# Optimization experiments

Measured on AMD Instinct MI355X. Metric: run time of the kernel, lower is better.

## Reference

```python
import jax, jax.numpy as jnp
import numpy as np


def setup_inputs() -> dict:
    key = jax.random.key(0)
    ks = jax.random.split(key, 7)
    B, C, H, W = 8, 1024, 64, 64
    heads, head_dim, red = 8, 128, 8
    s = 1.0 / np.sqrt(head_dim)
    return {
        "x": jax.random.normal(ks[0], (B, C, H, W), jnp.float32),
        "Wq": jax.random.normal(ks[1], (heads, red, head_dim), jnp.float32) * s,
        "bq": jax.random.normal(ks[2], (heads, red), jnp.float32) * s,
        "Wk": jax.random.normal(ks[3], (heads, red, head_dim), jnp.float32) * s,
        "bk": jax.random.normal(ks[4], (heads, red), jnp.float32) * s,
        "Wv": jax.random.normal(ks[5], (heads, head_dim, head_dim), jnp.float32) * s,
        "bv": jax.random.normal(ks[6], (heads, head_dim), jnp.float32) * s,
    }


def reference(x, Wq, bq, Wk, bk, Wv, bv):
    B, C, H, W = x.shape
    heads, red, d = Wq.shape  # d = head_dim
    # (B, heads, head_dim, HW)
    xh = x.reshape(B, heads, d, H * W)
    # per-head spatial average pool: (B, heads, head_dim)
    avg = jnp.mean(xh, axis=-1)
    # torch Linear: y = x @ W.T + b, applied per head
    q = jnp.einsum("bhds,hrd->bhsr", xh, Wq) + bq[None, :, None, :]   # (B,H,S,r)
    k = jnp.einsum("bhd,hrd->bhr", avg, Wk) + bk[None]                 # (B,H,r)
    v = jnp.einsum("bhd,hed->bhe", avg, Wv) + bv[None]                 # (B,H,d)
    # single-key attention; softmax over the spatial dim (torch dim=1)
    scores = jnp.einsum("bhsr,bhr->bhs", q, k)                          # (B,H,S)
    attn = jax.nn.softmax(scores, axis=-1)
    out = jnp.einsum("bhs,bhe->bhes", attn, v)                          # (B,H,d,S)
    return out.reshape(B, C, H, W)
```

## Files before the change

### kernel.cpp

```cpp
#include <hip/hip_runtime.h>
#include <math.h>

#define SDIM 4096
#define DDIM 128
#define RED 8
#define BATCH 8
#define BH 64
#define CH 1024

typedef float vfloat4 __attribute__((ext_vector_type(4)));

#define WS_V   8192
#define WS_SC  16384

__inline__ __device__ float wave_reduce_sum(float v) {
#pragma unroll
    for (int o = 32; o > 0; o >>= 1) v += __shfl_down(v, o, 64);
    return v;
}
__inline__ __device__ float wave_reduce_max(float v) {
#pragma unroll
    for (int o = 32; o > 0; o >>= 1) v = fmaxf(v, __shfl_down(v, o, 64));
    return v;
}

__global__ __launch_bounds__(256) void k_avg(const float* __restrict__ x,
                                             float* __restrict__ ws) {
    const int row = blockIdx.x;
    const int t = threadIdx.x;
    const float4* xr = (const float4*)(x + (size_t)row * SDIM);
    float s = 0.f;
#pragma unroll
    for (int p = 0; p < 4; ++p) {
        float4 v = xr[t + 256 * p];
        s += v.x + v.y + v.z + v.w;
    }
    s = wave_reduce_sum(s);
    __shared__ float part[4];
    const int wave = t >> 6, lane = t & 63;
    if (lane == 0) part[wave] = s;
    __syncthreads();
    if (t == 0) {
        float tot = part[0] + part[1] + part[2] + part[3];
        ws[row] = tot * (1.0f / SDIM);
    }
}

__global__ __launch_bounds__(256) void k_scores(
        const float* __restrict__ x,
        const float* __restrict__ Wq, const float* __restrict__ bq,
        const float* __restrict__ Wk, const float* __restrict__ bk,
        float* __restrict__ ws) {
    const int blk = blockIdx.x;
    const int bh = blk >> 3, chunk = blk & 7;
    const int b = bh >> 3, h = bh & 7;
    const int t = threadIdx.x;

    __shared__ float avgs[DDIM];
    __shared__ float kk[RED];
    __shared__ float wqs[DDIM];
    __shared__ float cc;

    if (t < DDIM) avgs[t] = ws[b * CH + h * DDIM + t];
    __syncthreads();
    if (t < RED) {
        const float* wkr = Wk + (h * RED + t) * DDIM;
        float acc = 0.f;
#pragma unroll 8
        for (int d = 0; d < DDIM; ++d) acc += wkr[d] * avgs[d];
        kk[t] = acc + bk[h * RED + t];
    }
    __syncthreads();
    if (t < DDIM) {
        float acc = 0.f;
#pragma unroll
        for (int r = 0; r < RED; ++r) acc += Wq[(h * RED + r) * DDIM + t] * kk[r];
        wqs[t] = acc;
    }
    if (t == 0) {
        float acc = 0.f;
#pragma unroll
        for (int r = 0; r < RED; ++r) acc += bq[h * RED + r] * kk[r];
        cc = acc;
    }
    __syncthreads();

    const int s0 = chunk * 512 + t * 2;
    const float* xb = x + (size_t)(b * CH + h * DDIM) * SDIM + s0;
    float2 acc;
    const float c = cc;
    acc.x = c; acc.y = c;
#pragma unroll 16
    for (int d = 0; d < DDIM; ++d) {
        float2 xv = *(const float2*)(xb + (size_t)d * SDIM);
        const float w = wqs[d];
        acc.x += xv.x * w; acc.y += xv.y * w;
    }
    *(float2*)(ws + WS_SC + (size_t)bh * SDIM + s0) = acc;
}

__global__ __launch_bounds__(256) void k_softmax_v(
        const float* __restrict__ Wv, const float* __restrict__ bv,
        float* __restrict__ ws) {
    const int bh = blockIdx.x;
    const int b = bh >> 3, h = bh & 7;
    const int t = threadIdx.x;

    __shared__ float avgs[DDIM];
    if (t < DDIM) avgs[t] = ws[b * CH + h * DDIM + t];
    __syncthreads();
    if (t < DDIM) {
        const float* wvr = Wv + (h * DDIM + t) * DDIM;
        float acc = 0.f;
#pragma unroll 8
        for (int d = 0; d < DDIM; ++d) acc += wvr[d] * avgs[d];
        ws[WS_V + bh * DDIM + t] = acc + bv[h * DDIM + t];
    }

    float4* sc = (float4*)(ws + WS_SC + (size_t)bh * SDIM);
    float4 vals[4];
    float m = -1e30f;
#pragma unroll
    for (int p = 0; p < 4; ++p) {
        vals[p] = sc[t + 256 * p];
        m = fmaxf(m, fmaxf(fmaxf(vals[p].x, vals[p].y), fmaxf(vals[p].z, vals[p].w)));
    }
    m = wave_reduce_max(m);
    __shared__ float smax[4];
    __shared__ float ssum[4];
    const int wave = t >> 6, lane = t & 63;
    if (lane == 0) smax[wave] = m;
    __syncthreads();
    const float gm = fmaxf(fmaxf(smax[0], smax[1]), fmaxf(smax[2], smax[3]));
    float sum = 0.f;
#pragma unroll
    for (int p = 0; p < 4; ++p) {
        vals[p].x = expf(vals[p].x - gm);
        vals[p].y = expf(vals[p].y - gm);
        vals[p].z = expf(vals[p].z - gm);
        vals[p].w = expf(vals[p].w - gm);
        sum += vals[p].x + vals[p].y + vals[p].z + vals[p].w;
    }
    sum = wave_reduce_sum(sum);
    if (lane == 0) ssum[wave] = sum;
    __syncthreads();
    const float inv = 1.0f / (ssum[0] + ssum[1] + ssum[2] + ssum[3]);
#pragma unroll
    for (int p = 0; p < 4; ++p) {
        float4 o;
        o.x = vals[p].x * inv; o.y = vals[p].y * inv;
        o.z = vals[p].z * inv; o.w = vals[p].w * inv;
        sc[t + 256 * p] = o;
    }
}

__global__ __launch_bounds__(256) void k_out(const float* __restrict__ ws,
                                             float* __restrict__ out) {
    const vfloat4* attn = (const vfloat4*)(ws + WS_SC);
    const float* vv = ws + WS_V;
    const size_t total = (size_t)BATCH * CH * (SDIM / 4);
    const size_t stride = (size_t)gridDim.x * blockDim.x;
    for (size_t f = (size_t)blockIdx.x * blockDim.x + threadIdx.x; f < total; f += stride) {
        const int s4 = (int)(f & 1023);
        const int ce = (int)((f >> 10) & 1023);
        const int b = (int)(f >> 20);
        const int bh = (b << 3) | (ce >> 7);
        const int e = ce & 127;
        const vfloat4 a = attn[bh * 1024 + s4];
        const float vx = vv[bh * 128 + e];
        vfloat4 o = a * vx;
        __builtin_nontemporal_store(o, ((vfloat4*)out) + f);
    }
}

extern "C" void kernel_launch(void* const* d_in, const int* in_sizes, int n_in,
                              void* d_out, int out_size, void* d_ws, size_t ws_size,
                              hipStream_t stream) {
    const float* x  = (const float*)d_in[0];
    const float* Wq = (const float*)d_in[1];
    const float* bq = (const float*)d_in[2];
    const float* bk = (const float*)d_in[4];
    const float* Wk = (const float*)d_in[3];
    const float* Wv = (const float*)d_in[5];
    const float* bv = (const float*)d_in[6];
    float* out = (float*)d_out;
    float* ws  = (float*)d_ws;

    k_avg<<<8192, 256, 0, stream>>>(x, ws);
    k_scores<<<512, 256, 0, stream>>>(x, Wq, bq, Wk, bk, ws);
    k_softmax_v<<<BH, 256, 0, stream>>>(Wv, bv, ws);
    k_out<<<8192, 256, 0, stream>>>(ws, out);
}
```

Measured before the change: 269.3 us.

## Fuse all stages into one cooperative persistent kernel with grid syncs

Replaces the four separate kernel launches with a single cooperative kernel of 256 blocks that runs the average pool, the k/v/wq projections, the scores, the softmax and the output broadcast, separated by grid.sync barriers. Intermediates are staged in the workspace at new offsets. This removes launch gaps between stages, but only 64 blocks do work in the projection and softmax phases, the grid barriers cost time, and the bandwidth-bound stages run with fewer blocks in flight. If the cooperative launch fails, it falls back to the old four-kernel path.

```diff
diff --git a/kernel.cpp b/kernel.cpp
--- a/kernel.cpp
+++ b/kernel.cpp
@@ -1,5 +1,8 @@
 #include <hip/hip_runtime.h>
+#include <hip/hip_cooperative_groups.h>
 #include <math.h>
+
+namespace cg = cooperative_groups;
 
 #define SDIM 4096
 #define DDIM 128
@@ -8,10 +11,15 @@
 #define BH 64
 #define CH 1024
 
+#define NBLK 256
+#define NTHR 512
+
 typedef float vfloat4 __attribute__((ext_vector_type(4)));
 
-#define WS_V   8192
-#define WS_SC  16384
+#define WS_WQ  8192
+#define WS_V   16384
+#define WS_C   24576
+#define WS_SC  32768
 
 __inline__ __device__ float wave_reduce_sum(float v) {
 #pragma unroll
@@ -22,6 +30,151 @@
 #pragma unroll
     for (int o = 32; o > 0; o >>= 1) v = fmaxf(v, __shfl_down(v, o, 64));
     return v;
+}
+
+__global__ __launch_bounds__(NTHR, 2) void k_fused(
+        const float* __restrict__ x,
+        const float* __restrict__ Wq, const float* __restrict__ bq,
+        const float* __restrict__ Wk, const float* __restrict__ bk,
+        const float* __restrict__ Wv, const float* __restrict__ bv,
+        float* __restrict__ out, float* __restrict__ ws) {
+    cg::grid_group grid = cg::this_grid();
+    const int blk = blockIdx.x;
+    const int t = threadIdx.x;
+    const int wave = t >> 6, lane = t & 63;
+
+#pragma unroll
+    for (int r = 0; r < 4; ++r) {
+        const int row = blk * 32 + wave * 4 + r;
+        const float4* xr = (const float4*)(x + (size_t)row * SDIM);
+        float s = 0.f;
+#pragma unroll
+        for (int p = 0; p < 16; ++p) {
+            float4 v = xr[lane + 64 * p];
+            s += (v.x + v.y) + (v.z + v.w);
+        }
+        s = wave_reduce_sum(s);
+        if (lane == 0) ws[row] = s * (1.0f / SDIM);
+    }
+    grid.sync();
+
+    __shared__ float avgs[DDIM];
+    __shared__ float kk[RED];
+    __shared__ float wqs[DDIM];
+    __shared__ float cc;
+    __shared__ float smax[8];
+    __shared__ float ssum[8];
+
+    if (blk < BH) {
+        const int b = blk >> 3, h = blk & 7;
+        if (t < DDIM) avgs[t] = ws[b * CH + h * DDIM + t];
+        __syncthreads();
+        if (t < RED) {
+            const float* wkr = Wk + (h * RED + t) * DDIM;
+            float acc = 0.f;
+#pragma unroll 8
+            for (int d = 0; d < DDIM; ++d) acc += wkr[d] * avgs[d];
+            kk[t] = acc + bk[h * RED + t];
+        }
+        __syncthreads();
+        if (t < DDIM) {
+            float acc = 0.f;
+#pragma unroll
+            for (int r = 0; r < RED; ++r) acc += Wq[(h * RED + r) * DDIM + t] * kk[r];
+            ws[WS_WQ + blk * DDIM + t] = acc;
+            const float* wvr = Wv + (h * DDIM + t) * DDIM;
+            float vacc = 0.f;
+#pragma unroll 8
+            for (int d = 0; d < DDIM; ++d) vacc += wvr[d] * avgs[d];
+            ws[WS_V + blk * DDIM + t] = vacc + bv[h * DDIM + t];
+        }
+        if (t == 0) {
+            float acc = 0.f;
+#pragma unroll
+            for (int r = 0; r < RED; ++r) acc += bq[h * RED + r] * kk[r];
+            ws[WS_C + blk] = acc;
+        }
+    }
+    grid.sync();
+
+    {
+        const int bh = blk >> 2, chunk = blk & 3;
+        const int b = bh >> 3, h = bh & 7;
+        if (t < DDIM) wqs[t] = ws[WS_WQ + bh * DDIM + t];
+        if (t == 0) cc = ws[WS_C + bh];
+        __syncthreads();
+        const int s0 = chunk * 1024 + t * 2;
+        const float* xb = x + (size_t)(b * CH + h * DDIM) * SDIM + s0;
+        const float c = cc;
+        float2 acc; acc.x = c; acc.y = c;
+#pragma unroll 16
+        for (int d = 0; d < DDIM; ++d) {
+            float2 xv = *(const float2*)(xb + (size_t)d * SDIM);
+            const float w = wqs[d];
+            acc.x += xv.x * w; acc.y += xv.y * w;
+        }
+        *(float2*)(ws + WS_SC + (size_t)bh * SDIM + s0) = acc;
+    }
+    grid.sync();
+
+    if (blk < BH) {
+        float4* sc = (float4*)(ws + WS_SC + (size_t)blk * SDIM);
+        float4 vals[2];
+        float m = -1e30f;
+#pragma unroll
+        for (int p = 0; p < 2; ++p) {
+            vals[p] = sc[t + NTHR * p];
+            m = fmaxf(m, fmaxf(fmaxf(vals[p].x, vals[p].y), fmaxf(vals[p].z, vals[p].w)));
+        }
+        m = wave_reduce_max(m);
+        if (lane == 0) smax[wave] = m;
+        __syncthreads();
+        float gm = smax[0];
+#pragma unroll
+        for (int w2 = 1; w2 < 8; ++w2) gm = fmaxf(gm, smax[w2]);
+        float sum = 0.f;
+#pragma unroll
+        for (int p = 0; p < 2; ++p) {
+            vals[p].x = expf(vals[p].x - gm);
+            vals[p].y = expf(vals[p].y - gm);
+            vals[p].z = expf(vals[p].z - gm);
+            vals[p].w = expf(vals[p].w - gm);
+            sum += vals[p].x + vals[p].y + vals[p].z + vals[p].w;
+        }
+        sum = wave_reduce_sum(sum);
+        if (lane == 0) ssum[wave] = sum;
+        __syncthreads();
+        float tot = ssum[0];
+#pragma unroll
+        for (int w2 = 1; w2 < 8; ++w2) tot += ssum[w2];
+        const float inv = 1.0f / tot;
+#pragma unroll
+        for (int p = 0; p < 2; ++p) {
+            float4 o;
+            o.x = vals[p].x * inv; o.y = vals[p].y * inv;
+            o.z = vals[p].z * inv; o.w = vals[p].w * inv;
+            sc[t + NTHR * p] = o;
+        }
+    }
+    grid.sync();
+
+    {
+        const vfloat4* attn = (const vfloat4*)(ws + WS_SC);
+        const float* vv = ws + WS_V;
+        const size_t total = (size_t)BATCH * CH * (SDIM / 4);
+        const size_t stride = (size_t)NBLK * NTHR;
+        for (size_t f = (size_t)blk * NTHR + t; f < total; f += stride) {
+            const int s4 = (int)(f & 1023);
+            const int ce = (int)((f >> 10) & 1023);
+            const int b = (int)(f >> 20);
+            const int bh = (b << 3) | (ce >> 7);
+            const int e = ce & 127;
+            const vfloat4 a = attn[bh * 1024 + s4];
+            const float vx = vv[bh * 128 + e];
+            vfloat4 o = a * vx;
+            __builtin_nontemporal_store(o, ((vfloat4*)out) + f);
+        }
+    }
 }
 
 __global__ __launch_bounds__(256) void k_avg(const float* __restrict__ x,
@@ -40,10 +193,7 @@
     const int wave = t >> 6, lane = t & 63;
     if (lane == 0) part[wave] = s;
     __syncthreads();
-    if (t == 0) {
-        float tot = part[0] + part[1] + part[2] + part[3];
-        ws[row] = tot * (1.0f / SDIM);
-    }
+    if (t == 0) ws[row] = (part[0] + part[1] + part[2] + part[3]) * (1.0f / SDIM);
 }
 
 __global__ __launch_bounds__(256) void k_scores(
@@ -55,12 +205,10 @@
     const int bh = blk >> 3, chunk = blk & 7;
     const int b = bh >> 3, h = bh & 7;
     const int t = threadIdx.x;
-
     __shared__ float avgs[DDIM];
     __shared__ float kk[RED];
     __shared__ float wqs[DDIM];
     __shared__ float cc;
-
     if (t < DDIM) avgs[t] = ws[b * CH + h * DDIM + t];
     __syncthreads();
     if (t < RED) {
@@ -84,7 +232,6 @@
         cc = acc;
     }
     __syncthreads();
-
     const int s0 = chunk * 512 + t * 2;
     const float* xb = x + (size_t)(b * CH + h * DDIM) * SDIM + s0;
     float2 acc;
@@ -105,7 +252,6 @@
     const int bh = blockIdx.x;
     const int b = bh >> 3, h = bh & 7;
     const int t = threadIdx.x;
-
     __shared__ float avgs[DDIM];
     if (t < DDIM) avgs[t] = ws[b * CH + h * DDIM + t];
     __syncthreads();
@@ -116,7 +262,6 @@
         for (int d = 0; d < DDIM; ++d) acc += wvr[d] * avgs[d];
         ws[WS_V + bh * DDIM + t] = acc + bv[h * DDIM + t];
     }
-
     float4* sc = (float4*)(ws + WS_SC + (size_t)bh * SDIM);
     float4 vals[4];
     float m = -1e30f;
@@ -179,15 +324,21 @@
     const float* x  = (const float*)d_in[0];
     const float* Wq = (const float*)d_in[1];
     const float* bq = (const float*)d_in[2];
+    const float* Wk = (const float*)d_in[3];
     const float* bk = (const float*)d_in[4];
-    const float* Wk = (const float*)d_in[3];
     const float* Wv = (const float*)d_in[5];
     const float* bv = (const float*)d_in[6];
     float* out = (float*)d_out;
     float* ws  = (float*)d_ws;
 
-    k_avg<<<8192, 256, 0, stream>>>(x, ws);
-    k_scores<<<512, 256, 0, stream>>>(x, Wq, bq, Wk, bk, ws);
-    k_softmax_v<<<BH, 256, 0, stream>>>(Wv, bv, ws);
-    k_out<<<8192, 256, 0, stream>>>(ws, out);
-}
+    void* args[] = { (void*)&x, (void*)&Wq, (void*)&bq, (void*)&Wk, (void*)&bk,
+                     (void*)&Wv, (void*)&bv, (void*)&out, (void*)&ws };
+    hipError_t err = hipLaunchCooperativeKernel((const void*)k_fused, dim3(NBLK),
+                                                dim3(NTHR), args, 0, stream);
+    if (err != hipSuccess) {
+        k_avg<<<8192, 256, 0, stream>>>(x, ws);
+        k_scores<<<512, 256, 0, stream>>>(x, Wq, bq, Wk, bk, ws);
+        k_softmax_v<<<BH, 256, 0, stream>>>(Wv, bv, ws);
+        k_out<<<8192, 256, 0, stream>>>(ws, out);
+    }
+}
```

Measured after the change: 407.8 us. 1.51x slower.
